# Optimization experiments

Measured on AMD Instinct MI355X. Metric: run time of the kernel, lower is better.

Reference implementation:

```python
import jax, jax.numpy as jnp
import numpy as np

SHIFT = 1  # fixed choice for the random +/-1 shift_direction in the torch module


def setup_inputs() -> dict:
    key = jax.random.key(0)
    kx, kw = jax.random.split(key)
    x = jax.random.normal(kx, (128, 128, 56, 56), dtype=jnp.float32)
    W = jax.random.normal(kw, (32, 3, 2, 3, 4), dtype=jnp.float32)
    return {"x": x, "W": W}


def reference(x, W):
    n = x.shape[0]
    # sum-pool over a factor-2 split of the channel dim: (n,128,56,56)->(n,64,56,56)
    t = x.reshape(n, 2, 64, 56, 56).sum(axis=1)
    # view channels as (32 groups, 2): (n,32,2,56,56)
    t = t.reshape(n, 32, 2, 56, 56)
    # first torch unfold == size-3 zero-padded window along the 32-group axis
    tp = jnp.pad(t, ((0, 0), (1, 1), (0, 0), (0, 0), (0, 0)))
    w1 = jnp.stack([tp[:, i:i + 32] for i in range(3)], axis=1)  # (n,3,32,2,56,56)
    # circular shift along the last spatial axis (torch.roll on dim 5)
    w1 = jnp.roll(w1, SHIFT, axis=5)
    # second torch unfold == size-3 zero-padded window along the rolled 56 axis
    wp = jnp.pad(w1, ((0, 0), (0, 0), (0, 0), (0, 0), (0, 0), (1, 1)))
    w2 = jnp.stack([wp[..., l:l + 56] for l in range(3)], axis=5)  # (n,3,32,2,56,3,56)
    # grouped local-conv contraction; axes: n,i=win1(3),j=32,m=2,p=56,l=win2(3),o=56; k=4
    out = jnp.einsum('nijmplo,jimlk->njpok', w2, W)  # (n,32,56,56,4)
    t5 = out.transpose(0, 2, 3, 1, 4).reshape(n, 56, 56, 128)
    t5 = jnp.roll(t5, SHIFT, axis=1)  # roll along first spatial axis
    return t5.transpose(0, 3, 1, 2)  # (n,128,56,56)
```

## Files before the change

### kernel.cpp

```cpp
#include <hip/hip_runtime.h>

#define TPB 256

__global__ __launch_bounds__(TPB, 4) void fused_shift_conv(const float* __restrict__ x,
                                                           const float* __restrict__ Wg,
                                                           float* __restrict__ out) {
    const int bid = blockIdx.x;
    const int p = bid % 56;
    const int n = bid / 56;
    const int P = (p + 55) % 56;

    __shared__ float4 sm4[128 * 15];

    const int tid = threadIdx.x;
    const int h = tid & 1;
    const int c = tid >> 1;
    const int j = c >> 2;
    const int k = c & 3;

    float wt[3][2][3];
#pragma unroll
    for (int i = 0; i < 3; ++i)
#pragma unroll
        for (int m = 0; m < 2; ++m)
#pragma unroll
            for (int l = 0; l < 3; ++l)
                wt[i][m][l] = Wg[(((j * 3 + i) * 2 + m) * 3 + l) * 4 + k];

    {
        const float4* x4 = reinterpret_cast<const float4*>(x);
#pragma unroll
        for (int it = 0; it < 4; ++it) {
            const int idx = tid + it * TPB;
            if (idx < 896) {
                const int r = idx / 14;
                const int v = idx - r * 14;
                const size_t base = (size_t)(n * 128 + r) * 784 + (size_t)P * 14 + (size_t)v;
                const float4 a = x4[base];
                const float4 b = x4[base + (size_t)64 * 784];
                float4 s;
                s.x = a.x + b.x; s.y = a.y + b.y; s.z = a.z + b.z; s.w = a.w + b.w;
                sm4[r * 15 + v] = s;
            }
        }
    }
    __syncthreads();

    const int q0 = h ? 6 : 13;
    const int qb = h ? 6 : -1;

    float acc[28];
#pragma unroll
    for (int u = 0; u < 28; ++u) acc[u] = 0.f;

#pragma unroll
    for (int i = 0; i < 3; ++i) {
        const int g = j + i - 1;
        if ((unsigned)g < 32u) {
#pragma unroll
            for (int m = 0; m < 2; ++m) {
                const float4* row4 = &sm4[(2 * g + m) * 15];
                float fe[32];
                {
                    const float4 t = row4[q0];
                    fe[0] = t.x; fe[1] = t.y; fe[2] = t.z; fe[3] = t.w;
                }
#pragma unroll
                for (int q = 1; q < 8; ++q) {
                    const float4 t = row4[qb + q];
                    fe[4 * q + 0] = t.x; fe[4 * q + 1] = t.y;
                    fe[4 * q + 2] = t.z; fe[4 * q + 3] = t.w;
                }
                float va[30];
#pragma unroll
                for (int d = 0; d < 30; ++d) va[d] = fe[d + 2];
                va[0]  = h ? va[0] : 0.f;
                va[29] = h ? 0.f : va[29];

                const float w0 = wt[i][m][0];
                const float w1 = wt[i][m][1];
                const float w2 = wt[i][m][2];
#pragma unroll
                for (int u = 0; u < 28; ++u)
                    acc[u] += w0 * va[u] + w1 * va[u + 1] + w2 * va[u + 2];
            }
        }
    }

    __syncthreads();
#pragma unroll
    for (int u4 = 0; u4 < 7; ++u4) {
        float4 v4;
        v4.x = acc[4 * u4 + 0];
        v4.y = acc[4 * u4 + 1];
        v4.z = acc[4 * u4 + 2];
        v4.w = acc[4 * u4 + 3];
        sm4[c * 15 + h * 7 + u4] = v4;
    }
    __syncthreads();
    float4* o4 = reinterpret_cast<float4*>(out);
#pragma unroll
    for (int it = 0; it < 7; ++it) {
        const int idx = tid + it * TPB;
        const int ch = idx / 14;
        const int v = idx - ch * 14;
        o4[(size_t)(n * 128 + ch) * 784 + (size_t)p * 14 + (size_t)v] = sm4[ch * 15 + v];
    }
}

extern "C" void kernel_launch(void* const* d_in, const int* in_sizes, int n_in,
                              void* d_out, int out_size, void* d_ws, size_t ws_size,
                              hipStream_t stream) {
    const float* x = (const float*)d_in[0];
    const float* W = (const float*)d_in[1];
    float* out = (float*)d_out;
    const int n = in_sizes[0] / (128 * 56 * 56);
    const int grid = n * 56;
    fused_shift_conv<<<grid, TPB, 0, stream>>>(x, W, out);
}
```

Baseline: 114.8 us.

## Process two output rows per block with 512 threads

Each block now computes two adjacent output rows (p0, p0+1) with 512 threads instead of one row with 256, halving the grid. The shared buffer holds the two channel-summed input rows interleaved, and each output row is read from its own rolled input row. Output is written back through shared memory in two channel halves, so each channel's store covers two contiguous rows. The aim is fewer blocks and longer contiguous writes, at the cost of an extra sync round and a tighter launch-bounds occupancy hint that may raise register pressure.

```diff
diff --git a/kernel.cpp b/kernel.cpp
--- a/kernel.cpp
+++ b/kernel.cpp
@@ -1,20 +1,24 @@
 #include <hip/hip_runtime.h>
 
-#define TPB 256
+#define TPB 512
 
-__global__ __launch_bounds__(TPB, 4) void fused_shift_conv(const float* __restrict__ x,
+__global__ __launch_bounds__(TPB, 8) void fused_shift_conv(const float* __restrict__ x,
                                                            const float* __restrict__ Wg,
                                                            float* __restrict__ out) {
     const int bid = blockIdx.x;
-    const int p = bid % 56;
-    const int n = bid / 56;
-    const int P = (p + 55) % 56;
+    const int ptile = bid % 28;
+    const int n = bid / 28;
+    const int p0 = ptile * 2;
+    const int P0 = (p0 + 55) % 56;
+    const int P1 = p0;
 
     __shared__ float4 sm4[128 * 15];
 
     const int tid = threadIdx.x;
-    const int h = tid & 1;
-    const int c = tid >> 1;
+    const int pl = tid >> 8;
+    const int t8 = tid & 255;
+    const int h = t8 & 1;
+    const int c = t8 >> 1;
     const int j = c >> 2;
     const int k = c & 3;
 
@@ -32,15 +36,18 @@
 #pragma unroll
         for (int it = 0; it < 4; ++it) {
             const int idx = tid + it * TPB;
-            if (idx < 896) {
-                const int r = idx / 14;
-                const int v = idx - r * 14;
-                const size_t base = (size_t)(n * 128 + r) * 784 + (size_t)P * 14 + (size_t)v;
+            if (idx < 1792) {
+                const int S = idx / 14;
+                const int v = idx - S * 14;
+                const int r = S >> 1;
+                const int q = S & 1;
+                const int Pq = q ? P1 : P0;
+                const size_t base = (size_t)(n * 128 + r) * 784 + (size_t)Pq * 14 + (size_t)v;
                 const float4 a = x4[base];
                 const float4 b = x4[base + (size_t)64 * 784];
                 float4 s;
                 s.x = a.x + b.x; s.y = a.y + b.y; s.z = a.z + b.z; s.w = a.w + b.w;
-                sm4[r * 15 + v] = s;
+                sm4[S * 15 + v] = s;
             }
         }
     }
@@ -59,7 +66,7 @@
         if ((unsigned)g < 32u) {
 #pragma unroll
             for (int m = 0; m < 2; ++m) {
-                const float4* row4 = &sm4[(2 * g + m) * 15];
+                const float4* row4 = &sm4[((2 * g + m) * 2 + pl) * 15];
                 float fe[32];
                 {
                     const float4 t = row4[q0];
@@ -87,24 +94,37 @@
         }
     }
 
-    __syncthreads();
+    const int chalf = c >> 6;
+    const int cr = c & 63;
+    float4* o4 = reinterpret_cast<float4*>(out);
+
 #pragma unroll
-    for (int u4 = 0; u4 < 7; ++u4) {
-        float4 v4;
-        v4.x = acc[4 * u4 + 0];
-        v4.y = acc[4 * u4 + 1];
-        v4.z = acc[4 * u4 + 2];
-        v4.w = acc[4 * u4 + 3];
-        sm4[c * 15 + h * 7 + u4] = v4;
-    }
-    __syncthreads();
-    float4* o4 = reinterpret_cast<float4*>(out);
+    for (int half = 0; half < 2; ++half) {
+        __syncthreads();
+        if (chalf == half) {
 #pragma unroll
-    for (int it = 0; it < 7; ++it) {
-        const int idx = tid + it * TPB;
-        const int ch = idx / 14;
-        const int v = idx - ch * 14;
-        o4[(size_t)(n * 128 + ch) * 784 + (size_t)p * 14 + (size_t)v] = sm4[ch * 15 + v];
+            for (int u4 = 0; u4 < 7; ++u4) {
+                float4 v4;
+                v4.x = acc[4 * u4 + 0];
+                v4.y = acc[4 * u4 + 1];
+                v4.z = acc[4 * u4 + 2];
+                v4.w = acc[4 * u4 + 3];
+                sm4[(cr + 64 * pl) * 15 + h * 7 + u4] = v4;
+            }
+        }
+        __syncthreads();
+#pragma unroll
+        for (int it = 0; it < 4; ++it) {
+            const int idx = tid + it * TPB;
+            if (idx < 1792) {
+                const int chp = idx / 14;
+                const int v = idx - chp * 14;
+                const int scr = chp & 63;
+                const int spl = chp >> 6;
+                o4[(size_t)(n * 128 + half * 64 + scr) * 784 + (size_t)(p0 + spl) * 14 + (size_t)v] =
+                    sm4[chp * 15 + v];
+            }
+        }
     }
 }
 
@@ -115,6 +135,6 @@
     const float* W = (const float*)d_in[1];
     float* out = (float*)d_out;
     const int n = in_sizes[0] / (128 * 56 * 56);
-    const int grid = n * 56;
+    const int grid = n * 28;
     fused_shift_conv<<<grid, TPB, 0, stream>>>(x, W, out);
 }
```

Result: slower. 138.5 us (+20.7%).
